# Optimization experiments

Measured on AMD Instinct MI355X. Metric: run time of the kernel, lower is better.

## Reference

```python
import jax, jax.numpy as jnp
import numpy as np
from jax import lax

ALPHA = 2.0
EROSIONS = 10


def setup_inputs() -> dict:
    key = jax.random.key(0)
    k1, k2 = jax.random.split(key)
    B, C, H, W = 32, 1, 1024, 1024
    pred = jax.random.uniform(k1, (B, C, H, W), dtype=jnp.float32)
    target = jax.random.uniform(k2, (B, C, H, W), dtype=jnp.float32)
    return {"pred": pred, "target": target}


def _hausdorff_er_loss(pred, target):
    # 3x3 cross structuring element * 0.2 (sums to 1), as in kernel2D
    kernel = jnp.array([[0.0, 0.2, 0.0],
                        [0.2, 0.2, 0.2],
                        [0.0, 0.2, 0.0]], dtype=pred.dtype)
    kernel = kernel[None, None]  # OIHW: (1,1,3,3)

    bound = (pred - target) ** 2  # (B,1,H,W)

    def step(carry, k):
        b, acc = carry
        # scipy.ndimage.convolve(mode='constant', cval=0) == SAME zero-padded conv;
        # the cross kernel is symmetric so correlation == convolution.
        dil = lax.conv_general_dilated(
            b, kernel, window_strides=(1, 1), padding='SAME',
            dimension_numbers=('NCHW', 'OIHW', 'NCHW'))
        er = jnp.maximum(dil - 0.5, 0.0)
        # per-sample min/max normalization (ptp over the whole (1,H,W) array)
        emin = er.min(axis=(1, 2, 3), keepdims=True)
        emax = er.max(axis=(1, 2, 3), keepdims=True)
        ptp = emax - emin
        er = jnp.where(ptp > 0, (er - emin) / jnp.where(ptp > 0, ptp, 1.0), er)
        acc = acc + er * (k + 1.0) ** ALPHA
        return (er, acc), None

    ks = jnp.arange(EROSIONS, dtype=bound.dtype)
    (_, eroted), _ = lax.scan(step, (bound, jnp.zeros_like(bound)), ks)
    return eroted.mean()


def reference(pred, target):
    return _hausdorff_er_loss(pred, target)
```

## Files before the change

kernel.cpp:

```cpp
#include <hip/hip_runtime.h>

#define BATCH 32
#define HH 1024
#define WW 1024
#define NPIX (HH * WW)
#define NEROS 10
#define TPS 64
#define NTILES (BATCH * TPS)
#define T0R 8
#define T0PS 128
#define NT0 (BATCH * T0PS)
#define FWPS 32

__device__ __forceinline__ float4 ld4f(const float* p) {
    return *reinterpret_cast<const float4*>(p);
}

__global__ __launch_bounds__(512, 8) void conv0_kernel(
    const float* __restrict__ pred, const float* __restrict__ tgt,
    float* __restrict__ out, unsigned* __restrict__ Fout,
    unsigned* __restrict__ cntOut, unsigned* __restrict__ omin,
    unsigned* __restrict__ omax, double* __restrict__ osum) {
    int blk = blockIdx.x;
    blk = (blk & 7) * (NT0 >> 3) + (blk >> 3);
    const int s = blk >> 7, ty = blk & 127, ry = ty << 3;
    const int tid = threadIdx.x, lane = tid & 63, w = tid >> 6;
    const size_t sbase = (size_t)s * NPIX;

    __shared__ float sb[10 * 1024];

    float4 pv[5], tv[5];
#pragma unroll
    for (int i = 0; i < 5; ++i) {
        const int slot = tid + 512 * i;
        const int y = ry - 1 + (slot >> 8);
        if (y >= 0 && y < HH) {
            const size_t idx = sbase + (size_t)y * WW + ((slot & 255) << 2);
            pv[i] = ld4f(pred + idx);
            tv[i] = ld4f(tgt + idx);
        } else {
            pv[i] = make_float4(0.f, 0.f, 0.f, 0.f);
            tv[i] = make_float4(0.f, 0.f, 0.f, 0.f);
        }
    }
#pragma unroll
    for (int i = 0; i < 5; ++i) {
        const int slot = tid + 512 * i;
        float4 b;
        b.x = (pv[i].x - tv[i].x) * (pv[i].x - tv[i].x);
        b.y = (pv[i].y - tv[i].y) * (pv[i].y - tv[i].y);
        b.z = (pv[i].z - tv[i].z) * (pv[i].z - tv[i].z);
        b.w = (pv[i].w - tv[i].w) * (pv[i].w - tv[i].w);
        *reinterpret_cast<float4*>(
            &sb[(slot >> 8) * 1024 + ((slot & 255) << 2)]) = b;
    }
    __syncthreads();

    float lmin = 3.4e38f, lmax = 0.f, lsum = 0.f;
    unsigned rowbits = 0u;
    {
        const int y = ry + w;
        float O[16];
        bool nz = false;
#pragma unroll
        for (int q = 0; q < 4; ++q) {
            const int xw = (q << 8) + (lane << 2);
            const float4 U = *(const float4*)&sb[w * 1024 + xw];
            const float4 Cc = *(const float4*)&sb[(w + 1) * 1024 + xw];
            const float4 D = *(const float4*)&sb[(w + 2) * 1024 + xw];
            float lf = __shfl_up(Cc.w, 1);
            if (lane == 0)
                lf = (q > 0) ? sb[(w + 1) * 1024 + (q << 8) - 1] : 0.f;
            float rt = __shfl_down(Cc.x, 1);
            if (lane == 63)
                rt = (q < 3) ? sb[(w + 1) * 1024 + (q << 8) + 256] : 0.f;
            const float cv[4] = {Cc.x, Cc.y, Cc.z, Cc.w};
            const float uv[4] = {U.x, U.y, U.z, U.w};
            const float dv[4] = {D.x, D.y, D.z, D.w};
            const float lvv[4] = {lf, Cc.x, Cc.y, Cc.z};
            const float rvv[4] = {Cc.y, Cc.z, Cc.w, rt};
#pragma unroll
            for (int j = 0; j < 4; ++j) {
                const float conv =
                    0.2f * (uv[j] + dv[j] + cv[j] + lvv[j] + rvv[j]);
                const float er = fmaxf(conv - 0.5f, 0.f);
                O[(q << 2) + j] = er;
                lmin = fminf(lmin, er);
                lmax = fmaxf(lmax, er);
                lsum += er;
                nz = nz || (er > 0.f);
            }
        }
        if (__ballot(nz) != 0ull) {
            const size_t ob = sbase + (size_t)y * WW;
#pragma unroll
            for (int q = 0; q < 4; ++q)
                *reinterpret_cast<float4*>(out + ob + (q << 8) + (lane << 2)) =
                    make_float4(O[q << 2], O[(q << 2) + 1], O[(q << 2) + 2],
                                O[(q << 2) + 3]);
            rowbits = 1u << w;
        }
    }

#pragma unroll
    for (int off = 32; off > 0; off >>= 1) {
        lmin = fminf(lmin, __shfl_down(lmin, off));
        lmax = fmaxf(lmax, __shfl_down(lmax, off));
        lsum += __shfl_down(lsum, off);
    }
    __shared__ float smn[8], smx[8], ssm[8];
    __shared__ unsigned sfb[8];
    if (lane == 0) {
        smn[w] = lmin;
        smx[w] = lmax;
        ssm[w] = lsum;
        sfb[w] = rowbits;
    }
    __syncthreads();
    if (tid == 0) {
        unsigned fmask = sfb[0];
        float bmn = smn[0], bmx = smx[0], bsm = ssm[0];
#pragma unroll
        for (int i = 1; i < 8; ++i) {
            bmn = fminf(bmn, smn[i]);
            bmx = fmaxf(bmx, smx[i]);
            bsm += ssm[i];
            fmask |= sfb[i];
        }
        if (fmask) {
            atomicOr(&Fout[s * FWPS + (ty >> 2)], fmask << ((ty & 3) * 8));
            atomicAdd(cntOut, 1u);
        }
        atomicMin(&omin[s], __float_as_uint(bmn));
        if (bmx > 0.f) atomicMax(&omax[s], __float_as_uint(bmx));
        if (bsm > 0.f) atomicAdd(&osum[s], (double)bsm);
    }
}

__global__ __launch_bounds__(256, 4) void convt_kernel(
    const float* __restrict__ in, float* __restrict__ out,
    const unsigned* __restrict__ Fprev, unsigned* __restrict__ Fout,
    const unsigned* __restrict__ cntPrev, unsigned* __restrict__ cntOut,
    const unsigned* __restrict__ pmin, const unsigned* __restrict__ pmax,
    unsigned* __restrict__ omin, unsigned* __restrict__ omax,
    double* __restrict__ osum) {
    if (*cntPrev == 0u) return;

    int blk = blockIdx.x;
    blk = (blk & 7) * (NTILES >> 3) + (blk >> 3);
    const int s = blk >> 6, ty = blk & 63, ry = ty << 4;
    const int tid = threadIdx.x, lane = tid & 63, w = tid >> 6;
    const int xb = lane << 4;
    const size_t sbase = (size_t)s * NPIX;

    const unsigned* Fs = Fprev + s * FWPS;
    const int w32 = ty >> 1, sh = (ty & 1) * 16;
    const unsigned cur = Fs[w32];
    unsigned M = ((cur >> sh) & 0xFFFFu) << 1;
    if (ty > 0)
        M |= (ty & 1) ? ((cur >> 15) & 1u) : ((Fs[w32 - 1] >> 31) & 1u);
    if (ty < TPS - 1) {
        const unsigned nb = (ty & 1) ? (Fs[w32 + 1] & 1u) : ((cur >> 16) & 1u);
        M |= nb << 17;
    }
    if (M == 0u) {
        if (tid == 0) atomicMin(&omin[s], 0u);
        return;
    }

    float a = 1.f, cc = 0.f;
    {
        const float mn = __uint_as_float(pmin[s]);
        const float mx = __uint_as_float(pmax[s]);
        const float ptp = mx - mn;
        if (ptp > 0.f) { a = 1.f / ptp; cc = mn; }
    }

    const int r0 = w << 2;
    float A[16], B[16], C[16], O[16];

    auto loadRow = [&](int y, float* V) {
        const bool ok =
            (y >= 0 && y < HH) && (((M >> (y - ry + 1)) & 1u) != 0u);
        if (!ok) {
#pragma unroll
            for (int j = 0; j < 16; ++j) V[j] = 0.f;
            return;
        }
        const size_t idx = sbase + (size_t)y * WW + xb;
#pragma unroll
        for (int q = 0; q < 4; ++q) {
            const float4 v = ld4f(in + idx + 4 * q);
            V[4 * q + 0] = v.x;
            V[4 * q + 1] = v.y;
            V[4 * q + 2] = v.z;
            V[4 * q + 3] = v.w;
        }
    };

    loadRow(ry + r0 - 1, A);
    loadRow(ry + r0, B);

    float lmin = 3.4e38f, lmax = 0.f, lsum = 0.f;
    unsigned rowbits = 0u;

#pragma unroll
    for (int r = 0; r < 4; ++r) {
        const int y = ry + r0 + r;
        loadRow(y + 1, C);
        const bool act = (((M >> (r0 + r)) & 7u) != 0u);
        if (act) {
            float lfe = __shfl_up(B[15], 1);
            if (lane == 0) lfe = 0.f;
            float rte = __shfl_down(B[0], 1);
            if (lane == 63) rte = 0.f;
            const float vert =
                1.f + (y > 0 ? 1.f : 0.f) + (y < HH - 1 ? 1.f : 0.f);
            bool nz = false;
#pragma unroll
            for (int j = 0; j < 16; ++j) {
                const float lf = (j == 0) ? lfe : B[j - 1];
                const float rt = (j == 15) ? rte : B[j + 1];
                const float conv = 0.2f * (A[j] + C[j] + B[j] + lf + rt);
                const int x = xb + j;
                const float kf = 0.2f * (vert + (x > 0 ? 1.f : 0.f) +
                                         (x < WW - 1 ? 1.f : 0.f));
                const float dil = (conv - cc * kf) * a;
                const float er = fmaxf(dil - 0.5f, 0.f);
                O[j] = er;
                lmin = fminf(lmin, er);
                lmax = fmaxf(lmax, er);
                lsum += er;
                nz = nz || (er > 0.f);
            }
            if (__ballot(nz) != 0ull) {
                const size_t oidx = sbase + (size_t)y * WW + xb;
#pragma unroll
                for (int q = 0; q < 4; ++q)
                    *reinterpret_cast<float4*>(out + oidx + 4 * q) =
                        make_float4(O[4 * q], O[4 * q + 1], O[4 * q + 2],
                                    O[4 * q + 3]);
                rowbits |= 1u << (r0 + r);
            }
        } else {
            lmin = fminf(lmin, 0.f);
        }
#pragma unroll
        for (int j = 0; j < 16; ++j) {
            A[j] = B[j];
            B[j] = C[j];
        }
    }

#pragma unroll
    for (int off = 32; off > 0; off >>= 1) {
        lmin = fminf(lmin, __shfl_down(lmin, off));
        lmax = fmaxf(lmax, __shfl_down(lmax, off));
        lsum += __shfl_down(lsum, off);
    }
    __shared__ float smn[4], smx[4], ssm[4];
    __shared__ unsigned sfb[4];
    if (lane == 0) {
        smn[w] = lmin;
        smx[w] = lmax;
        ssm[w] = lsum;
        sfb[w] = rowbits;
    }
    __syncthreads();
    if (tid == 0) {
        const unsigned fmask = sfb[0] | sfb[1] | sfb[2] | sfb[3];
        float bmn = smn[0], bmx = smx[0], bsm = ssm[0];
#pragma unroll
        for (int i = 1; i < 4; ++i) {
            bmn = fminf(bmn, smn[i]);
            bmx = fmaxf(bmx, smx[i]);
            bsm += ssm[i];
        }
        if (fmask) {
            atomicOr(&Fout[s * FWPS + w32], fmask << sh);
            atomicAdd(cntOut, 1u);
        }
        atomicMin(&omin[s], __float_as_uint(bmn));
        if (bmx > 0.f) atomicMax(&omax[s], __float_as_uint(bmx));
        if (bsm > 0.f) atomicAdd(&osum[s], (double)bsm);
    }
}

__global__ void init_kernel(unsigned* __restrict__ minb,
                            unsigned* __restrict__ maxb,
                            double* __restrict__ sums,
                            unsigned* __restrict__ F,
                            unsigned* __restrict__ cnt) {
    const int i = blockIdx.x * blockDim.x + threadIdx.x;
    if (i < NEROS * BATCH) {
        minb[i] = 0x7f800000u;
        maxb[i] = 0u;
        sums[i] = 0.0;
    }
    if (i < NEROS * BATCH * FWPS) F[i] = 0u;
    if (i < NEROS) cnt[i] = 0u;
}

__global__ void final_kernel(const unsigned* __restrict__ minb,
                             const unsigned* __restrict__ maxb,
                             const double* __restrict__ sums,
                             float* __restrict__ out) {
    const int s = threadIdx.x;
    double tot = 0.0;
    if (s < BATCH) {
        for (int k = 0; k < NEROS; ++k) {
            const float mn = __uint_as_float(minb[k * BATCH + s]);
            const float mx = __uint_as_float(maxb[k * BATCH + s]);
            const double sm = sums[k * BATCH + s];
            const float ptp = mx - mn;
            double v;
            if (ptp > 0.f)
                v = (sm - (double)NPIX * (double)mn) / (double)ptp;
            else
                v = sm;
            tot += (double)((k + 1) * (k + 1)) * v;
        }
    }
#pragma unroll
    for (int off = 32; off > 0; off >>= 1) tot += __shfl_down(tot, off);
    if (s == 0) out[0] = (float)(tot / ((double)BATCH * (double)NPIX));
}

extern "C" void kernel_launch(void* const* d_in, const int* in_sizes, int n_in,
                              void* d_out, int out_size, void* d_ws,
                              size_t ws_size, hipStream_t stream) {
    const float* pred = (const float*)d_in[0];
    const float* tgt = (const float*)d_in[1];
    float* out = (float*)d_out;

    float* buf0 = (float*)d_ws;
    float* buf1 = buf0 + (size_t)BATCH * NPIX;
    unsigned* minb = (unsigned*)(buf1 + (size_t)BATCH * NPIX);
    unsigned* maxb = minb + NEROS * BATCH;
    double* sums = (double*)(maxb + NEROS * BATCH);
    unsigned* F = (unsigned*)(sums + NEROS * BATCH);
    unsigned* cnt = F + (size_t)NEROS * BATCH * FWPS;

    init_kernel<<<40, 256, 0, stream>>>(minb, maxb, sums, F, cnt);

    conv0_kernel<<<NT0, 512, 0, stream>>>(pred, tgt, buf0, F, &cnt[0], minb,
                                          maxb, sums);

    float* bufs[2] = {buf0, buf1};
    for (int k = 1; k < NEROS; ++k) {
        const float* src = bufs[(k - 1) & 1];
        float* dst = bufs[k & 1];
        convt_kernel<<<NTILES, 256, 0, stream>>>(
            src, dst, F + (size_t)(k - 1) * BATCH * FWPS,
            F + (size_t)k * BATCH * FWPS, &cnt[k - 1], &cnt[k],
            minb + (size_t)(k - 1) * BATCH, maxb + (size_t)(k - 1) * BATCH,
            minb + (size_t)k * BATCH, maxb + (size_t)k * BATCH,
            sums + (size_t)k * BATCH);
    }

    final_kernel<<<1, 64, 0, stream>>>(minb, maxb, sums, out);
}
```

Baseline: 140.5 us.

## Stream 64-row slabs through a shared-memory ring buffer in conv0

conv0 now processes a 64-row slab per block using an 18-row ring buffer in shared memory, prefetching the next 8 input rows into registers while computing the current 8. This cuts redundant halo-row reads of pred/target and reduces per-block reduction atomics, and writes flag words directly instead of atomicOr. In exchange the grid shrinks to 512 large blocks with more LDS each, lowering occupancy and adding per-step barriers.

Result: faster. 137.6 us (-2.0%).

```diff
diff --git a/kernel.cpp b/kernel.cpp
--- a/kernel.cpp
+++ b/kernel.cpp
@@ -7,99 +7,153 @@
 #define NEROS 10
 #define TPS 64
 #define NTILES (BATCH * TPS)
-#define T0R 8
-#define T0PS 128
-#define NT0 (BATCH * T0PS)
 #define FWPS 32
+#define NB0 512
+#define SLOTS 18
 
 __device__ __forceinline__ float4 ld4f(const float* p) {
     return *reinterpret_cast<const float4*>(p);
 }
 
-__global__ __launch_bounds__(512, 8) void conv0_kernel(
+__global__ __launch_bounds__(512, 2) void conv0_kernel(
     const float* __restrict__ pred, const float* __restrict__ tgt,
     float* __restrict__ out, unsigned* __restrict__ Fout,
     unsigned* __restrict__ cntOut, unsigned* __restrict__ omin,
     unsigned* __restrict__ omax, double* __restrict__ osum) {
     int blk = blockIdx.x;
-    blk = (blk & 7) * (NT0 >> 3) + (blk >> 3);
-    const int s = blk >> 7, ty = blk & 127, ry = ty << 3;
+    blk = (blk & 7) * (NB0 >> 3) + (blk >> 3);
+    const int s = blk >> 4, slab = blk & 15;
+    const int r0 = slab << 6;
     const int tid = threadIdx.x, lane = tid & 63, w = tid >> 6;
     const size_t sbase = (size_t)s * NPIX;
 
-    __shared__ float sb[10 * 1024];
-
-    float4 pv[5], tv[5];
-#pragma unroll
-    for (int i = 0; i < 5; ++i) {
-        const int slot = tid + 512 * i;
-        const int y = ry - 1 + (slot >> 8);
-        if (y >= 0 && y < HH) {
-            const size_t idx = sbase + (size_t)y * WW + ((slot & 255) << 2);
-            pv[i] = ld4f(pred + idx);
-            tv[i] = ld4f(tgt + idx);
-        } else {
-            pv[i] = make_float4(0.f, 0.f, 0.f, 0.f);
-            tv[i] = make_float4(0.f, 0.f, 0.f, 0.f);
-        }
-    }
-#pragma unroll
-    for (int i = 0; i < 5; ++i) {
-        const int slot = tid + 512 * i;
-        float4 b;
-        b.x = (pv[i].x - tv[i].x) * (pv[i].x - tv[i].x);
-        b.y = (pv[i].y - tv[i].y) * (pv[i].y - tv[i].y);
-        b.z = (pv[i].z - tv[i].z) * (pv[i].z - tv[i].z);
-        b.w = (pv[i].w - tv[i].w) * (pv[i].w - tv[i].w);
-        *reinterpret_cast<float4*>(
-            &sb[(slot >> 8) * 1024 + ((slot & 255) << 2)]) = b;
+    __shared__ float sb[SLOTS * 1024];
+    __shared__ float smn[8], smx[8], ssm[8];
+    __shared__ unsigned sfa[8], sfb[8];
+
+    {
+        float4 pv[5], tv[5];
+#pragma unroll
+        for (int i = 0; i < 5; ++i) {
+            const int idx = tid + 512 * i;
+            const int y = r0 - 1 + (idx >> 8);
+            if (y >= 0 && y < HH) {
+                const size_t g = sbase + (size_t)y * WW + ((idx & 255) << 2);
+                pv[i] = ld4f(pred + g);
+                tv[i] = ld4f(tgt + g);
+            } else {
+                pv[i] = make_float4(0.f, 0.f, 0.f, 0.f);
+                tv[i] = make_float4(0.f, 0.f, 0.f, 0.f);
+            }
+        }
+#pragma unroll
+        for (int i = 0; i < 5; ++i) {
+            const int idx = tid + 512 * i;
+            const int y = r0 - 1 + (idx >> 8);
+            const int slot = (int)((unsigned)(y + 1) % SLOTS);
+            float4 b;
+            b.x = (pv[i].x - tv[i].x) * (pv[i].x - tv[i].x);
+            b.y = (pv[i].y - tv[i].y) * (pv[i].y - tv[i].y);
+            b.z = (pv[i].z - tv[i].z) * (pv[i].z - tv[i].z);
+            b.w = (pv[i].w - tv[i].w) * (pv[i].w - tv[i].w);
+            *reinterpret_cast<float4*>(&sb[slot * 1024 + ((idx & 255) << 2)]) =
+                b;
+        }
     }
     __syncthreads();
 
     float lmin = 3.4e38f, lmax = 0.f, lsum = 0.f;
-    unsigned rowbits = 0u;
-    {
-        const int y = ry + w;
-        float O[16];
-        bool nz = false;
-#pragma unroll
-        for (int q = 0; q < 4; ++q) {
-            const int xw = (q << 8) + (lane << 2);
-            const float4 U = *(const float4*)&sb[w * 1024 + xw];
-            const float4 Cc = *(const float4*)&sb[(w + 1) * 1024 + xw];
-            const float4 D = *(const float4*)&sb[(w + 2) * 1024 + xw];
-            float lf = __shfl_up(Cc.w, 1);
-            if (lane == 0)
-                lf = (q > 0) ? sb[(w + 1) * 1024 + (q << 8) - 1] : 0.f;
-            float rt = __shfl_down(Cc.x, 1);
-            if (lane == 63)
-                rt = (q < 3) ? sb[(w + 1) * 1024 + (q << 8) + 256] : 0.f;
-            const float cv[4] = {Cc.x, Cc.y, Cc.z, Cc.w};
-            const float uv[4] = {U.x, U.y, U.z, U.w};
-            const float dv[4] = {D.x, D.y, D.z, D.w};
-            const float lvv[4] = {lf, Cc.x, Cc.y, Cc.z};
-            const float rvv[4] = {Cc.y, Cc.z, Cc.w, rt};
-#pragma unroll
-            for (int j = 0; j < 4; ++j) {
-                const float conv =
-                    0.2f * (uv[j] + dv[j] + cv[j] + lvv[j] + rvv[j]);
-                const float er = fmaxf(conv - 0.5f, 0.f);
-                O[(q << 2) + j] = er;
-                lmin = fminf(lmin, er);
-                lmax = fmaxf(lmax, er);
-                lsum += er;
-                nz = nz || (er > 0.f);
-            }
-        }
-        if (__ballot(nz) != 0ull) {
-            const size_t ob = sbase + (size_t)y * WW;
-#pragma unroll
-            for (int q = 0; q < 4; ++q)
-                *reinterpret_cast<float4*>(out + ob + (q << 8) + (lane << 2)) =
-                    make_float4(O[q << 2], O[(q << 2) + 1], O[(q << 2) + 2],
-                                O[(q << 2) + 3]);
-            rowbits = 1u << w;
-        }
+    unsigned fa = 0u, fb = 0u;
+
+    for (int t = 0; t < 8; ++t) {
+        const int rt = r0 + (t << 3);
+
+        float4 pv[4], tv[4];
+        if (t < 7) {
+#pragma unroll
+            for (int i = 0; i < 4; ++i) {
+                const int idx = tid + 512 * i;
+                const int y = rt + 9 + (idx >> 8);
+                if (y < HH) {
+                    const size_t g =
+                        sbase + (size_t)y * WW + ((idx & 255) << 2);
+                    pv[i] = ld4f(pred + g);
+                    tv[i] = ld4f(tgt + g);
+                } else {
+                    pv[i] = make_float4(0.f, 0.f, 0.f, 0.f);
+                    tv[i] = make_float4(0.f, 0.f, 0.f, 0.f);
+                }
+            }
+        }
+
+        {
+            const int y = rt + w;
+            const int sU = (int)((unsigned)y % SLOTS);
+            const int sC = (int)((unsigned)(y + 1) % SLOTS);
+            const int sD = (int)((unsigned)(y + 2) % SLOTS);
+            float O[16];
+            bool nz = false;
+#pragma unroll
+            for (int q = 0; q < 4; ++q) {
+                const int xw = (q << 8) + (lane << 2);
+                const float4 U = *(const float4*)&sb[sU * 1024 + xw];
+                const float4 Cc = *(const float4*)&sb[sC * 1024 + xw];
+                const float4 D = *(const float4*)&sb[sD * 1024 + xw];
+                float lf = __shfl_up(Cc.w, 1);
+                if (lane == 0)
+                    lf = (q > 0) ? sb[sC * 1024 + (q << 8) - 1] : 0.f;
+                float rt2 = __shfl_down(Cc.x, 1);
+                if (lane == 63)
+                    rt2 = (q < 3) ? sb[sC * 1024 + (q << 8) + 256] : 0.f;
+                const float cv[4] = {Cc.x, Cc.y, Cc.z, Cc.w};
+                const float uv[4] = {U.x, U.y, U.z, U.w};
+                const float dv[4] = {D.x, D.y, D.z, D.w};
+                const float lvv[4] = {lf, Cc.x, Cc.y, Cc.z};
+                const float rvv[4] = {Cc.y, Cc.z, Cc.w, rt2};
+#pragma unroll
+                for (int j = 0; j < 4; ++j) {
+                    const float conv =
+                        0.2f * (uv[j] + dv[j] + cv[j] + lvv[j] + rvv[j]);
+                    const float er = fmaxf(conv - 0.5f, 0.f);
+                    O[(q << 2) + j] = er;
+                    lmin = fminf(lmin, er);
+                    lmax = fmaxf(lmax, er);
+                    lsum += er;
+                    nz = nz || (er > 0.f);
+                }
+            }
+            if (__ballot(nz) != 0ull) {
+                const size_t ob = sbase + (size_t)y * WW;
+#pragma unroll
+                for (int q = 0; q < 4; ++q)
+                    *reinterpret_cast<float4*>(out + ob + (q << 8) +
+                                               (lane << 2)) =
+                        make_float4(O[q << 2], O[(q << 2) + 1],
+                                    O[(q << 2) + 2], O[(q << 2) + 3]);
+                const int ris = (t << 3) + w;
+                if (ris < 32)
+                    fa |= 1u << ris;
+                else
+                    fb |= 1u << (ris - 32);
+            }
+        }
+
+        if (t < 7) {
+#pragma unroll
+            for (int i = 0; i < 4; ++i) {
+                const int idx = tid + 512 * i;
+                const int y = rt + 9 + (idx >> 8);
+                const int slot = (int)((unsigned)(y + 1) % SLOTS);
+                float4 b;
+                b.x = (pv[i].x - tv[i].x) * (pv[i].x - tv[i].x);
+                b.y = (pv[i].y - tv[i].y) * (pv[i].y - tv[i].y);
+                b.z = (pv[i].z - tv[i].z) * (pv[i].z - tv[i].z);
+                b.w = (pv[i].w - tv[i].w) * (pv[i].w - tv[i].w);
+                *reinterpret_cast<float4*>(
+                    &sb[slot * 1024 + ((idx & 255) << 2)]) = b;
+            }
+        }
+        __syncthreads();
     }
 
 #pragma unroll
@@ -108,29 +162,28 @@
         lmax = fmaxf(lmax, __shfl_down(lmax, off));
         lsum += __shfl_down(lsum, off);
     }
-    __shared__ float smn[8], smx[8], ssm[8];
-    __shared__ unsigned sfb[8];
     if (lane == 0) {
         smn[w] = lmin;
         smx[w] = lmax;
         ssm[w] = lsum;
-        sfb[w] = rowbits;
+        sfa[w] = fa;
+        sfb[w] = fb;
     }
     __syncthreads();
     if (tid == 0) {
-        unsigned fmask = sfb[0];
+        unsigned fA = sfa[0], fB = sfb[0];
         float bmn = smn[0], bmx = smx[0], bsm = ssm[0];
 #pragma unroll
         for (int i = 1; i < 8; ++i) {
             bmn = fminf(bmn, smn[i]);
             bmx = fmaxf(bmx, smx[i]);
             bsm += ssm[i];
-            fmask |= sfb[i];
-        }
-        if (fmask) {
-            atomicOr(&Fout[s * FWPS + (ty >> 2)], fmask << ((ty & 3) * 8));
-            atomicAdd(cntOut, 1u);
-        }
+            fA |= sfa[i];
+            fB |= sfb[i];
+        }
+        Fout[s * FWPS + slab * 2] = fA;
+        Fout[s * FWPS + slab * 2 + 1] = fB;
+        if (fA | fB) atomicAdd(cntOut, 1u);
         atomicMin(&omin[s], __float_as_uint(bmn));
         if (bmx > 0.f) atomicMax(&omax[s], __float_as_uint(bmx));
         if (bsm > 0.f) atomicAdd(&osum[s], (double)bsm);
@@ -343,7 +396,7 @@
 
     init_kernel<<<40, 256, 0, stream>>>(minb, maxb, sums, F, cnt);
 
-    conv0_kernel<<<NT0, 512, 0, stream>>>(pred, tgt, buf0, F, &cnt[0], minb,
+    conv0_kernel<<<NB0, 512, 0, stream>>>(pred, tgt, buf0, F, &cnt[0], minb,
                                           maxb, sums);
 
     float* bufs[2] = {buf0, buf1};
```

## Track sparsity per 64-column chunk per row instead of per row

Applied to the files above, without the earlier changes.

Replaces the per-row activity bitmask with a 16-bit per-row mask recording which 64-pixel column chunks hold nonzero erosion values. Both kernels store and skip loads per chunk, so partially active rows move less memory. In exchange every row writes its own mask entry, each convt block stages the masks in shared memory with two extra barriers, and ballot post-processing adds work. Because skipped chunks are never written, correctness depends on neighbouring chunks of the previous buffer being zero-equivalent, which the mask must guarantee.

After: 122.5 us. 1.15x faster.

```diff
diff --git a/kernel.cpp b/kernel.cpp
--- a/kernel.cpp
+++ b/kernel.cpp
@@ -7,22 +7,21 @@
 #define NEROS 10
 #define TPS 64
 #define NTILES (BATCH * TPS)
-#define T0R 8
-#define T0PS 128
-#define NT0 (BATCH * T0PS)
-#define FWPS 32
+#define NB0 (BATCH * 128)
+#define FRPS 1024
 
 __device__ __forceinline__ float4 ld4f(const float* p) {
     return *reinterpret_cast<const float4*>(p);
 }
 
+
 __global__ __launch_bounds__(512, 8) void conv0_kernel(
     const float* __restrict__ pred, const float* __restrict__ tgt,
-    float* __restrict__ out, unsigned* __restrict__ Fout,
+    float* __restrict__ out, unsigned short* __restrict__ Fout,
     unsigned* __restrict__ cntOut, unsigned* __restrict__ omin,
     unsigned* __restrict__ omax, double* __restrict__ osum) {
     int blk = blockIdx.x;
-    blk = (blk & 7) * (NT0 >> 3) + (blk >> 3);
+    blk = (blk & 7) * (NB0 >> 3) + (blk >> 3);
     const int s = blk >> 7, ty = blk & 127, ry = ty << 3;
     const int tid = threadIdx.x, lane = tid & 63, w = tid >> 6;
     const size_t sbase = (size_t)s * NPIX;
@@ -57,50 +56,50 @@
     __syncthreads();
 
     float lmin = 3.4e38f, lmax = 0.f, lsum = 0.f;
-    unsigned rowbits = 0u;
-    {
-        const int y = ry + w;
-        float O[16];
+    unsigned rowmask = 0u;
+    const int y = ry + w;
+#pragma unroll
+    for (int q = 0; q < 4; ++q) {
+        const int xw = (q << 8) + (lane << 2);
+        const float4 U = *(const float4*)&sb[w * 1024 + xw];
+        const float4 Cc = *(const float4*)&sb[(w + 1) * 1024 + xw];
+        const float4 D = *(const float4*)&sb[(w + 2) * 1024 + xw];
+        float lf = __shfl_up(Cc.w, 1);
+        if (lane == 0) lf = (q > 0) ? sb[(w + 1) * 1024 + (q << 8) - 1] : 0.f;
+        float rt = __shfl_down(Cc.x, 1);
+        if (lane == 63)
+            rt = (q < 3) ? sb[(w + 1) * 1024 + (q << 8) + 256] : 0.f;
+        const float cv[4] = {Cc.x, Cc.y, Cc.z, Cc.w};
+        const float uv[4] = {U.x, U.y, U.z, U.w};
+        const float dv[4] = {D.x, D.y, D.z, D.w};
+        const float lvv[4] = {lf, Cc.x, Cc.y, Cc.z};
+        const float rvv[4] = {Cc.y, Cc.z, Cc.w, rt};
+        float O[4];
         bool nz = false;
 #pragma unroll
-        for (int q = 0; q < 4; ++q) {
-            const int xw = (q << 8) + (lane << 2);
-            const float4 U = *(const float4*)&sb[w * 1024 + xw];
-            const float4 Cc = *(const float4*)&sb[(w + 1) * 1024 + xw];
-            const float4 D = *(const float4*)&sb[(w + 2) * 1024 + xw];
-            float lf = __shfl_up(Cc.w, 1);
-            if (lane == 0)
-                lf = (q > 0) ? sb[(w + 1) * 1024 + (q << 8) - 1] : 0.f;
-            float rt = __shfl_down(Cc.x, 1);
-            if (lane == 63)
-                rt = (q < 3) ? sb[(w + 1) * 1024 + (q << 8) + 256] : 0.f;
-            const float cv[4] = {Cc.x, Cc.y, Cc.z, Cc.w};
-            const float uv[4] = {U.x, U.y, U.z, U.w};
-            const float dv[4] = {D.x, D.y, D.z, D.w};
-            const float lvv[4] = {lf, Cc.x, Cc.y, Cc.z};
-            const float rvv[4] = {Cc.y, Cc.z, Cc.w, rt};
-#pragma unroll
-            for (int j = 0; j < 4; ++j) {
-                const float conv =
-                    0.2f * (uv[j] + dv[j] + cv[j] + lvv[j] + rvv[j]);
-                const float er = fmaxf(conv - 0.5f, 0.f);
-                O[(q << 2) + j] = er;
-                lmin = fminf(lmin, er);
-                lmax = fmaxf(lmax, er);
-                lsum += er;
-                nz = nz || (er > 0.f);
-            }
-        }
-        if (__ballot(nz) != 0ull) {
-            const size_t ob = sbase + (size_t)y * WW;
-#pragma unroll
-            for (int q = 0; q < 4; ++q)
-                *reinterpret_cast<float4*>(out + ob + (q << 8) + (lane << 2)) =
-                    make_float4(O[q << 2], O[(q << 2) + 1], O[(q << 2) + 2],
-                                O[(q << 2) + 3]);
-            rowbits = 1u << w;
-        }
-    }
+        for (int j = 0; j < 4; ++j) {
+            const float conv = 0.2f * (uv[j] + dv[j] + cv[j] + lvv[j] + rvv[j]);
+            const float er = fmaxf(conv - 0.5f, 0.f);
+            O[j] = er;
+            lmin = fminf(lmin, er);
+            lmax = fmaxf(lmax, er);
+            lsum += er;
+            nz = nz || (er > 0.f);
+        }
+        const unsigned long long bal = __ballot(nz);
+        const bool myChunk =
+            ((bal >> ((lane >> 4) << 4)) & 0xFFFFull) != 0ull;
+        if (myChunk)
+            *reinterpret_cast<float4*>(out + sbase + (size_t)y * WW + xw) =
+                make_float4(O[0], O[1], O[2], O[3]);
+        unsigned g = 0;
+        if ((bal)&0xFFFFull) g |= 1u;
+        if ((bal >> 16) & 0xFFFFull) g |= 2u;
+        if ((bal >> 32) & 0xFFFFull) g |= 4u;
+        if ((bal >> 48) & 0xFFFFull) g |= 8u;
+        rowmask |= g << (q << 2);
+    }
+    if (lane == 0) Fout[s * FRPS + y] = (unsigned short)rowmask;
 
 #pragma unroll
     for (int off = 32; off > 0; off >>= 1) {
@@ -114,23 +113,20 @@
         smn[w] = lmin;
         smx[w] = lmax;
         ssm[w] = lsum;
-        sfb[w] = rowbits;
+        sfb[w] = rowmask;
     }
     __syncthreads();
     if (tid == 0) {
-        unsigned fmask = sfb[0];
+        unsigned any = sfb[0];
         float bmn = smn[0], bmx = smx[0], bsm = ssm[0];
 #pragma unroll
         for (int i = 1; i < 8; ++i) {
             bmn = fminf(bmn, smn[i]);
             bmx = fmaxf(bmx, smx[i]);
             bsm += ssm[i];
-            fmask |= sfb[i];
-        }
-        if (fmask) {
-            atomicOr(&Fout[s * FWPS + (ty >> 2)], fmask << ((ty & 3) * 8));
-            atomicAdd(cntOut, 1u);
-        }
+            any |= sfb[i];
+        }
+        if (any) atomicAdd(cntOut, 1u);
         atomicMin(&omin[s], __float_as_uint(bmn));
         if (bmx > 0.f) atomicMax(&omax[s], __float_as_uint(bmx));
         if (bsm > 0.f) atomicAdd(&osum[s], (double)bsm);
@@ -139,7 +135,7 @@
 
 __global__ __launch_bounds__(256, 4) void convt_kernel(
     const float* __restrict__ in, float* __restrict__ out,
-    const unsigned* __restrict__ Fprev, unsigned* __restrict__ Fout,
+    const unsigned short* __restrict__ Fprev, unsigned short* __restrict__ Fout,
     const unsigned* __restrict__ cntPrev, unsigned* __restrict__ cntOut,
     const unsigned* __restrict__ pmin, const unsigned* __restrict__ pmax,
     unsigned* __restrict__ omin, unsigned* __restrict__ omax,
@@ -153,17 +149,22 @@
     const int xb = lane << 4;
     const size_t sbase = (size_t)s * NPIX;
 
-    const unsigned* Fs = Fprev + s * FWPS;
-    const int w32 = ty >> 1, sh = (ty & 1) * 16;
-    const unsigned cur = Fs[w32];
-    unsigned M = ((cur >> sh) & 0xFFFFu) << 1;
-    if (ty > 0)
-        M |= (ty & 1) ? ((cur >> 15) & 1u) : ((Fs[w32 - 1] >> 31) & 1u);
-    if (ty < TPS - 1) {
-        const unsigned nb = (ty & 1) ? (Fs[w32 + 1] & 1u) : ((cur >> 16) & 1u);
-        M |= nb << 17;
-    }
-    if (M == 0u) {
+    __shared__ unsigned short sM[18];
+    __shared__ int sSkip;
+    if (tid < 18) {
+        const int yy = ry - 1 + tid;
+        sM[tid] =
+            (yy >= 0 && yy < HH) ? Fprev[s * FRPS + yy] : (unsigned short)0;
+    }
+    __syncthreads();
+    if (tid == 0) {
+        unsigned any = 0;
+#pragma unroll
+        for (int i = 0; i < 18; ++i) any |= sM[i];
+        sSkip = (any == 0u);
+    }
+    __syncthreads();
+    if (sSkip) {
         if (tid == 0) atomicMin(&omin[s], 0u);
         return;
     }
@@ -180,9 +181,8 @@
     float A[16], B[16], C[16], O[16];
 
     auto loadRow = [&](int y, float* V) {
-        const bool ok =
-            (y >= 0 && y < HH) && (((M >> (y - ry + 1)) & 1u) != 0u);
-        if (!ok) {
+        const unsigned mask = sM[y - ry + 1];
+        if (!((mask >> (lane >> 2)) & 1u)) {
 #pragma unroll
             for (int j = 0; j < 16; ++j) V[j] = 0.f;
             return;
@@ -202,13 +202,14 @@
     loadRow(ry + r0, B);
 
     float lmin = 3.4e38f, lmax = 0.f, lsum = 0.f;
-    unsigned rowbits = 0u;
+    unsigned blockAny = 0u;
 
 #pragma unroll
     for (int r = 0; r < 4; ++r) {
         const int y = ry + r0 + r;
         loadRow(y + 1, C);
-        const bool act = (((M >> (r0 + r)) & 7u) != 0u);
+        const int mi = r0 + r + 1;
+        const bool act = (sM[mi - 1] | sM[mi] | sM[mi + 1]) != 0;
         if (act) {
             float lfe = __shfl_up(B[15], 1);
             if (lane == 0) lfe = 0.f;
@@ -233,15 +234,21 @@
                 lsum += er;
                 nz = nz || (er > 0.f);
             }
-            if (__ballot(nz) != 0ull) {
+            const unsigned long long bal = __ballot(nz);
+            if (((bal >> ((lane >> 2) << 2)) & 0xFull) != 0ull) {
                 const size_t oidx = sbase + (size_t)y * WW + xb;
 #pragma unroll
                 for (int q = 0; q < 4; ++q)
                     *reinterpret_cast<float4*>(out + oidx + 4 * q) =
                         make_float4(O[4 * q], O[4 * q + 1], O[4 * q + 2],
                                     O[4 * q + 3]);
-                rowbits |= 1u << (r0 + r);
             }
+            unsigned rm = 0;
+#pragma unroll
+            for (int c = 0; c < 16; ++c)
+                if ((bal >> (c << 2)) & 0xFull) rm |= 1u << c;
+            if (lane == 0) Fout[s * FRPS + y] = (unsigned short)rm;
+            blockAny |= rm;
         } else {
             lmin = fminf(lmin, 0.f);
         }
@@ -264,11 +271,11 @@
         smn[w] = lmin;
         smx[w] = lmax;
         ssm[w] = lsum;
-        sfb[w] = rowbits;
+        sfb[w] = blockAny;
     }
     __syncthreads();
     if (tid == 0) {
-        const unsigned fmask = sfb[0] | sfb[1] | sfb[2] | sfb[3];
+        const unsigned any = sfb[0] | sfb[1] | sfb[2] | sfb[3];
         float bmn = smn[0], bmx = smx[0], bsm = ssm[0];
 #pragma unroll
         for (int i = 1; i < 4; ++i) {
@@ -276,10 +283,7 @@
             bmx = fmaxf(bmx, smx[i]);
             bsm += ssm[i];
         }
-        if (fmask) {
-            atomicOr(&Fout[s * FWPS + w32], fmask << sh);
-            atomicAdd(cntOut, 1u);
-        }
+        if (any) atomicAdd(cntOut, 1u);
         atomicMin(&omin[s], __float_as_uint(bmn));
         if (bmx > 0.f) atomicMax(&omax[s], __float_as_uint(bmx));
         if (bsm > 0.f) atomicAdd(&osum[s], (double)bsm);
@@ -289,7 +293,7 @@
 __global__ void init_kernel(unsigned* __restrict__ minb,
                             unsigned* __restrict__ maxb,
                             double* __restrict__ sums,
-                            unsigned* __restrict__ F,
+                            unsigned* __restrict__ F16u,
                             unsigned* __restrict__ cnt) {
     const int i = blockIdx.x * blockDim.x + threadIdx.x;
     if (i < NEROS * BATCH) {
@@ -297,7 +301,7 @@
         maxb[i] = 0u;
         sums[i] = 0.0;
     }
-    if (i < NEROS * BATCH * FWPS) F[i] = 0u;
+    if (i < NEROS * BATCH * FRPS / 2) F16u[i] = 0u;
     if (i < NEROS) cnt[i] = 0u;
 }
 
@@ -338,12 +342,12 @@
     unsigned* minb = (unsigned*)(buf1 + (size_t)BATCH * NPIX);
     unsigned* maxb = minb + NEROS * BATCH;
     double* sums = (double*)(maxb + NEROS * BATCH);
-    unsigned* F = (unsigned*)(sums + NEROS * BATCH);
-    unsigned* cnt = F + (size_t)NEROS * BATCH * FWPS;
-
-    init_kernel<<<40, 256, 0, stream>>>(minb, maxb, sums, F, cnt);
-
-    conv0_kernel<<<NT0, 512, 0, stream>>>(pred, tgt, buf0, F, &cnt[0], minb,
+    unsigned short* F = (unsigned short*)(sums + NEROS * BATCH);
+    unsigned* cnt = (unsigned*)(F + (size_t)NEROS * BATCH * FRPS);
+
+    init_kernel<<<640, 256, 0, stream>>>(minb, maxb, sums, (unsigned*)F, cnt);
+
+    conv0_kernel<<<NB0, 512, 0, stream>>>(pred, tgt, buf0, F, &cnt[0], minb,
                                           maxb, sums);
 
     float* bufs[2] = {buf0, buf1};
@@ -351,8 +355,8 @@
         const float* src = bufs[(k - 1) & 1];
         float* dst = bufs[k & 1];
         convt_kernel<<<NTILES, 256, 0, stream>>>(
-            src, dst, F + (size_t)(k - 1) * BATCH * FWPS,
-            F + (size_t)k * BATCH * FWPS, &cnt[k - 1], &cnt[k],
+            src, dst, F + (size_t)(k - 1) * BATCH * FRPS,
+            F + (size_t)k * BATCH * FRPS, &cnt[k - 1], &cnt[k],
             minb + (size_t)(k - 1) * BATCH, maxb + (size_t)(k - 1) * BATCH,
             minb + (size_t)k * BATCH, maxb + (size_t)k * BATCH,
             sums + (size_t)k * BATCH);
```
